# Optimization experiments

Measured on AMD Instinct MI355X. Metric: run time of the kernel, lower is better.

The kernel has to match this reference:

```python
import jax, jax.numpy as jnp
import numpy as np

D = 1024      # embedding_dimension
F = 4096      # intermediate_dimension
E = 8         # num_experts
K = 2         # top_k
B, S = 4, 2048


def setup_inputs() -> dict:
    key = jax.random.key(0)
    ks = jax.random.split(key, 6)
    scale_in = 1.0 / np.sqrt(D)
    scale_mid = 1.0 / np.sqrt(F)
    return {
        "x": jax.random.normal(ks[0], (B, S, D), dtype=jnp.float32),
        "router_w": jax.random.normal(ks[1], (E, D), dtype=jnp.float32) * scale_in,   # nn.Linear weight [out,in]
        "w1": jax.random.normal(ks[2], (E, F, D), dtype=jnp.float32) * scale_in,
        "b1": jax.random.normal(ks[3], (E, F), dtype=jnp.float32) * 0.01,
        "w2": jax.random.normal(ks[4], (E, D, F), dtype=jnp.float32) * scale_mid,
        "b2": jax.random.normal(ks[5], (E, D), dtype=jnp.float32) * 0.01,
    }


def reference(x, router_w, w1, b1, w2, b2):
    orig_shape = x.shape
    xf = x.reshape(-1, D)                                  # [T, D]
    logits = jnp.einsum("td,ed->te", xf, router_w)        # [T, E]
    top_vals, top_idx = jax.lax.top_k(logits, K)           # [T, K]
    probs = jax.nn.softmax(top_vals, axis=-1)              # [T, K]

    out = jnp.zeros_like(xf)
    for e in range(E):  # small fixed expert loop; masked dense combine
        # combine weight per token for expert e (0 if not routed)
        w = jnp.sum(jnp.where(top_idx == e, probs, 0.0), axis=-1)   # [T]
        h = jax.nn.gelu(jnp.einsum("td,fd->tf", xf, w1[e]) + b1[e], approximate=False)
        y = jnp.einsum("tf,df->td", h, w2[e]) + b2[e]
        out = out + w[:, None] * y
    return out.reshape(orig_shape)
```

## Files before the change

kernel.cpp:

```cpp
#include <hip/hip_runtime.h>
#include <hip/hip_bf16.h>
#include <stdint.h>

#define D 1024
#define F 4096
#define E 8
#define T 8192
#define SLOT_CAP 17408
#define BM 128
#define BK 32
#define EP_STRIDE 136

typedef __attribute__((ext_vector_type(8))) short bf16x8;
typedef __attribute__((ext_vector_type(4))) float f32x4;
typedef __attribute__((ext_vector_type(8))) unsigned short u16x8;

__device__ __forceinline__ unsigned short f2bf(float f) {
  unsigned u = __float_as_uint(f);
  u += 0x7fffu + ((u >> 16) & 1u);
  return (unsigned short)(u >> 16);
}
__device__ __forceinline__ float bf2f(unsigned short u) {
  return __uint_as_float(((unsigned)u) << 16);
}

__device__ __forceinline__ float gelu_f(float v) {
  float s = fabsf(v) * 0.70710678118654752f;
  float t = __builtin_amdgcn_rcpf(fmaf(0.3275911f, s, 1.0f));
  float p = fmaf(t, 1.061405429f, -1.453152027f);
  p = fmaf(t, p, 1.421413741f);
  p = fmaf(t, p, -0.284496736f);
  p = fmaf(t, p, 0.254829592f);
  p = p * t;
  float e = 1.0f - p * __expf(-s * s);
  e = copysignf(e, v);
  return 0.5f * v * (1.0f + e);
}

__device__ __forceinline__ void gload16(const void* g, void* l) {
  auto gp = (const __attribute__((address_space(1))) unsigned int*)(uintptr_t)g;
  auto lp = (__attribute__((address_space(3))) unsigned int*)(unsigned)(uintptr_t)l;
  __builtin_amdgcn_global_load_lds(gp, lp, 16, 0, 0);
}

__global__ __launch_bounds__(256) void prep_kernel(const float* __restrict__ x,
                                                   const float* __restrict__ rw,
                                                   const float* __restrict__ w1,
                                                   int* __restrict__ tok_e,
                                                   float* __restrict__ tok_p,
                                                   unsigned short* __restrict__ xg,
                                                   unsigned short* __restrict__ w1g) {
  if (blockIdx.x >= 2048) {
    int i = (blockIdx.x - 2048) * 256 + threadIdx.x;
    const float4* p = (const float4*)w1 + (size_t)i * 2;
    float4 a = p[0], b = p[1];
    u16x8 o;
    o[0] = f2bf(a.x); o[1] = f2bf(a.y); o[2] = f2bf(a.z); o[3] = f2bf(a.w);
    o[4] = f2bf(b.x); o[5] = f2bf(b.y); o[6] = f2bf(b.z); o[7] = f2bf(b.w);
    *(u16x8*)(w1g + (size_t)i * 8) = o;
    return;
  }
  int t = blockIdx.x * 4 + (threadIdx.x >> 6);
  int lane = threadIdx.x & 63;
  const float* xp = x + (size_t)t * D;
  unsigned short* xgp = xg + (size_t)t * D;
  double acc[E];
#pragma unroll
  for (int e = 0; e < E; e++) acc[e] = 0.0;
  for (int j = 0; j < D / 64; j++) {
    float xv = xp[j * 64 + lane];
    xgp[j * 64 + lane] = f2bf(xv);
#pragma unroll
    for (int e = 0; e < E; e++) acc[e] += (double)xv * (double)rw[e * D + j * 64 + lane];
  }
#pragma unroll
  for (int e = 0; e < E; e++) {
#pragma unroll
    for (int off = 32; off >= 1; off >>= 1) acc[e] += __shfl_xor(acc[e], off, 64);
  }
  if (lane == 0) {
    double v0 = -1e300, v1 = -1e300;
    int i0 = 0, i1 = 0;
#pragma unroll
    for (int e = 0; e < E; e++) {
      double v = acc[e];
      if (v > v0) { v1 = v0; i1 = i0; v0 = v; i0 = e; }
      else if (v > v1) { v1 = v; i1 = e; }
    }
    double e1 = exp(v1 - v0);
    double s = 1.0 + e1;
    tok_e[2 * t] = i0; tok_e[2 * t + 1] = i1;
    tok_p[2 * t] = (float)(1.0 / s);
    tok_p[2 * t + 1] = (float)(e1 / s);
  }
}

__global__ __launch_bounds__(64) void bucket_kernel(const int* __restrict__ tok_e,
                                                    int* __restrict__ perm,
                                                    int* __restrict__ slot_of,
                                                    int* __restrict__ counts,
                                                    int* __restrict__ offp) {
  const int e = blockIdx.x;
  const int lane = threadIdx.x;
  int cnt[E];
#pragma unroll
  for (int ee = 0; ee < E; ee++) cnt[ee] = 0;
  for (int idx = lane; idx < 2 * T; idx += 64) {
    int v = tok_e[idx];
#pragma unroll
    for (int ee = 0; ee < E; ee++) cnt[ee] += (v == ee) ? 1 : 0;
  }
#pragma unroll
  for (int ee = 0; ee < E; ee++) {
#pragma unroll
    for (int off = 32; off >= 1; off >>= 1) cnt[ee] += __shfl_xor(cnt[ee], off, 64);
  }
  int off_e[E + 1];
  int o = 0;
#pragma unroll
  for (int ee = 0; ee < E; ee++) { off_e[ee] = o; o += (cnt[ee] + (BM - 1)) & ~(BM - 1); }
  off_e[E] = o;
  if (e == 0 && lane == 0) {
#pragma unroll
    for (int ee = 0; ee < E; ee++) { counts[ee] = cnt[ee]; offp[ee] = off_e[ee]; }
    offp[E] = o;
  }
  int base = 0, mycnt = 0, myend = 0;
#pragma unroll
  for (int ee = 0; ee < E; ee++) {
    if (ee == e) { base = off_e[ee]; mycnt = cnt[ee]; myend = off_e[ee + 1]; }
  }
  const int pad0 = base + mycnt;
  for (int r = 0; r < 2 * T / 64; r++) {
    int idx = r * 64 + lane;
    int v = tok_e[idx];
    bool m = (v == e);
    unsigned long long mask = __ballot(m);
    int pre = __popcll(mask & ((1ull << lane) - 1ull));
    if (m) {
      int slot = base + pre;
      perm[slot] = idx >> 1;
      slot_of[idx] = slot;
    }
    base += __popcll(mask);
  }
  for (int i = pad0 + lane; i < myend; i += 64) perm[i] = 0;
}

__global__ __launch_bounds__(256, 4) void gemm1_kernel(const unsigned short* __restrict__ xg,
                                                       const unsigned short* __restrict__ w1g,
                                                       const float* __restrict__ b1,
                                                       const int* __restrict__ perm,
                                                       const int* __restrict__ offp,
                                                       const int* __restrict__ counts,
                                                       unsigned short* __restrict__ hbuf,
                                                       const float* __restrict__ w2,
                                                       unsigned short* __restrict__ w2g) {
  const int id = blockIdx.x;
  if (id >= 4352) {
    int i = (id - 4352) * 256 + threadIdx.x;
    const float4* p = (const float4*)w2 + (size_t)i * 2;
    float4 a = p[0], b = p[1];
    u16x8 o;
    o[0] = f2bf(a.x); o[1] = f2bf(a.y); o[2] = f2bf(a.z); o[3] = f2bf(a.w);
    o[4] = f2bf(b.x); o[5] = f2bf(b.y); o[6] = f2bf(b.z); o[7] = f2bf(b.w);
    *(u16x8*)(w2g + (size_t)i * 8) = o;
    return;
  }
  const int xcd = id & 7, loc = id >> 3;
  const int q = loc / 136, r = loc % 136;
  const int bm = xcd * 17 + (r >> 3);
  const int bn = q * 8 + (r & 7);
  const int row0 = bm * BM;
  if (row0 >= offp[E]) return;
  int e = 0;
#pragma unroll
  for (int i = 0; i < E; i++) if (row0 >= offp[i + 1]) e = i + 1;
  if (row0 >= offp[e] + counts[e]) return;

  const int tid = threadIdx.x, lane = tid & 63, w = tid >> 6;
  __shared__ __align__(16) unsigned short smem[BM * EP_STRIDE];
  unsigned short* As0 = smem;
  unsigned short* Bs0 = smem + 8192;

  const unsigned short* gsrc[4];
  unsigned short* ldst[4];
#pragma unroll
  for (int i = 0; i < 4; i++) {
    int ch = tid + 256 * i;
    if (ch < 512) {
      int ar = ch >> 2, ac = (ch & 3) * 8;
      gsrc[i] = xg + (size_t)perm[row0 + ar] * D + ac;
      ldst[i] = As0 + ch * 8;
    } else {
      int c = ch - 512;
      int br = c >> 2, bc = (c & 3) * 8;
      gsrc[i] = w1g + ((size_t)e * F + (size_t)bn * BM + br) * D + bc;
      ldst[i] = Bs0 + c * 8;
    }
  }
  auto stage = [&](int k0, int buf) {
#pragma unroll
    for (int i = 0; i < 4; i++) gload16(gsrc[i] + k0, ldst[i] + buf * (BM * BK));
  };

  f32x4 acc[4][4] = {};
  const int wr = (w >> 1) * 64, wc = (w & 1) * 64;
  const int fr = lane & 15, fq = lane >> 4;

  stage(0, 0);
  __syncthreads();
  int cur = 0;
  for (int k0 = 0; k0 < D; k0 += BK) {
    if (k0 + BK < D) stage(k0 + BK, cur ^ 1);
    bf16x8 a[4], b[4];
#pragma unroll
    for (int m = 0; m < 4; m++) a[m] = *(const bf16x8*)&As0[cur * 4096 + (wr + m * 16 + fr) * BK + fq * 8];
#pragma unroll
    for (int n = 0; n < 4; n++) b[n] = *(const bf16x8*)&Bs0[cur * 4096 + (wc + n * 16 + fr) * BK + fq * 8];
#pragma unroll
    for (int m = 0; m < 4; m++)
#pragma unroll
      for (int n = 0; n < 4; n++)
        acc[m][n] = __builtin_amdgcn_mfma_f32_16x16x32_bf16(a[m], b[n], acc[m][n], 0, 0, 0);
    __syncthreads();
    cur ^= 1;
  }

#pragma unroll
  for (int n = 0; n < 4; n++) {
    int cl = wc + n * 16 + fr;
    float bias = b1[e * F + bn * BM + cl];
#pragma unroll
    for (int m = 0; m < 4; m++) {
#pragma unroll
      for (int j = 0; j < 4; j++) {
        int rl = wr + m * 16 + fq * 4 + j;
        smem[rl * EP_STRIDE + cl] = f2bf(gelu_f(acc[m][n][j] + bias));
      }
    }
  }
  __syncthreads();
#pragma unroll
  for (int i = 0; i < 8; i++) {
    int idx = tid + i * 256;
    int r2 = idx >> 4, c = (idx & 15) * 8;
    u16x8 v = *(const u16x8*)&smem[r2 * EP_STRIDE + c];
    *(u16x8*)&hbuf[(size_t)(row0 + r2) * F + bn * BM + c] = v;
  }
}

__global__ __launch_bounds__(256, 4) void gemm2_kernel(const unsigned short* __restrict__ hbuf,
                                                       const unsigned short* __restrict__ w2g,
                                                       const float* __restrict__ b2,
                                                       const int* __restrict__ offp,
                                                       const int* __restrict__ counts,
                                                       unsigned short* __restrict__ ypart) {
  const int id = blockIdx.x;
  const int swz = (id & 7) * 272 + (id >> 3);
  const int bn = swz & 7;
  const int ks = (swz >> 3) & 1;
  const int bm = swz >> 4;
  const int row0 = bm * BM;
  if (row0 >= offp[E]) return;
  int e = 0;
#pragma unroll
  for (int i = 0; i < E; i++) if (row0 >= offp[i + 1]) e = i + 1;
  const int valid_end = offp[e] + counts[e];
  if (row0 >= valid_end) return;

  const int tid = threadIdx.x, lane = tid & 63, w = tid >> 6;
  __shared__ __align__(16) unsigned short smem[BM * EP_STRIDE];
  unsigned short* As0 = smem;
  unsigned short* Bs0 = smem + 8192;

  const int kbase = ks * (F / 2);
  const unsigned short* gsrc[4];
  unsigned short* ldst[4];
#pragma unroll
  for (int i = 0; i < 4; i++) {
    int ch = tid + 256 * i;
    if (ch < 512) {
      int ar = ch >> 2, ac = (ch & 3) * 8;
      gsrc[i] = hbuf + (size_t)(row0 + ar) * F + kbase + ac;
      ldst[i] = As0 + ch * 8;
    } else {
      int c = ch - 512;
      int br = c >> 2, bc = (c & 3) * 8;
      gsrc[i] = w2g + ((size_t)e * D + (size_t)bn * BM + br) * F + kbase + bc;
      ldst[i] = Bs0 + c * 8;
    }
  }
  auto stage = [&](int k0, int buf) {
#pragma unroll
    for (int i = 0; i < 4; i++) gload16(gsrc[i] + k0, ldst[i] + buf * (BM * BK));
  };

  f32x4 acc[4][4] = {};
  const int wr = (w >> 1) * 64, wc = (w & 1) * 64;
  const int fr = lane & 15, fq = lane >> 4;

  stage(0, 0);
  __syncthreads();
  int cur = 0;
  for (int k0 = 0; k0 < F / 2; k0 += BK) {
    if (k0 + BK < F / 2) stage(k0 + BK, cur ^ 1);
    bf16x8 a[4], b[4];
#pragma unroll
    for (int m = 0; m < 4; m++) a[m] = *(const bf16x8*)&As0[cur * 4096 + (wr + m * 16 + fr) * BK + fq * 8];
#pragma unroll
    for (int n = 0; n < 4; n++) b[n] = *(const bf16x8*)&Bs0[cur * 4096 + (wc + n * 16 + fr) * BK + fq * 8];
#pragma unroll
    for (int m = 0; m < 4; m++)
#pragma unroll
      for (int n = 0; n < 4; n++)
        acc[m][n] = __builtin_amdgcn_mfma_f32_16x16x32_bf16(a[m], b[n], acc[m][n], 0, 0, 0);
    __syncthreads();
    cur ^= 1;
  }

#pragma unroll
  for (int n = 0; n < 4; n++) {
    int cl = wc + n * 16 + fr;
    float bias = (ks == 0) ? b2[e * D + bn * BM + cl] : 0.0f;
#pragma unroll
    for (int m = 0; m < 4; m++) {
#pragma unroll
      for (int j = 0; j < 4; j++) {
        int rl = wr + m * 16 + fq * 4 + j;
        smem[rl * EP_STRIDE + cl] = f2bf(acc[m][n][j] + bias);
      }
    }
  }
  __syncthreads();
  unsigned short* ybase = ypart + (size_t)ks * SLOT_CAP * D;
#pragma unroll
  for (int i = 0; i < 8; i++) {
    int idx = tid + i * 256;
    int r2 = idx >> 4, c = (idx & 15) * 8;
    if (row0 + r2 < valid_end) {
      u16x8 v = *(const u16x8*)&smem[r2 * EP_STRIDE + c];
      *(u16x8*)&ybase[(size_t)(row0 + r2) * D + bn * BM + c] = v;
    }
  }
}

__global__ __launch_bounds__(256) void combine_kernel(const unsigned short* __restrict__ ypart,
                                                      const int* __restrict__ slot_of,
                                                      const float* __restrict__ tok_p,
                                                      float* __restrict__ out) {
  int i = blockIdx.x * 256 + threadIdx.x;
  int t = i >> 7;
  int g8 = i & 127;
  int s0 = slot_of[2 * t], s1 = slot_of[2 * t + 1];
  float g0 = tok_p[2 * t], g1 = tok_p[2 * t + 1];
  const unsigned short* p0 = ypart;
  const unsigned short* p1 = ypart + (size_t)SLOT_CAP * D;
  u16x8 a0 = *(const u16x8*)(p0 + (size_t)s0 * D + g8 * 8);
  u16x8 b0 = *(const u16x8*)(p1 + (size_t)s0 * D + g8 * 8);
  u16x8 a1 = *(const u16x8*)(p0 + (size_t)s1 * D + g8 * 8);
  u16x8 b1 = *(const u16x8*)(p1 + (size_t)s1 * D + g8 * 8);
  float o[8];
#pragma unroll
  for (int j = 0; j < 8; j++)
    o[j] = g0 * (bf2f(a0[j]) + bf2f(b0[j])) + g1 * (bf2f(a1[j]) + bf2f(b1[j]));
  float4* op = (float4*)(out + (size_t)t * D + g8 * 8);
  op[0] = make_float4(o[0], o[1], o[2], o[3]);
  op[1] = make_float4(o[4], o[5], o[6], o[7]);
}

extern "C" void kernel_launch(void* const* d_in, const int* in_sizes, int n_in,
                              void* d_out, int out_size, void* d_ws, size_t ws_size,
                              hipStream_t stream) {
  const float* x = (const float*)d_in[0];
  const float* rw = (const float*)d_in[1];
  const float* w1 = (const float*)d_in[2];
  const float* b1 = (const float*)d_in[3];
  const float* w2 = (const float*)d_in[4];
  const float* b2 = (const float*)d_in[5];
  float* out = (float*)d_out;

  char* ws = (char*)d_ws;
  size_t off = 0;
  auto alloc = [&](size_t bytes) {
    void* p = ws + off;
    off = (off + bytes + 255) & ~(size_t)255;
    return p;
  };
  int* counts = (int*)alloc(E * 4);
  int* offp = (int*)alloc((E + 1) * 4);
  int* tok_e = (int*)alloc((size_t)T * 2 * 4);
  float* tok_p = (float*)alloc((size_t)T * 2 * 4);
  int* perm = (int*)alloc((size_t)SLOT_CAP * 4);
  int* slot_of = (int*)alloc((size_t)T * 2 * 4);
  unsigned short* xg = (unsigned short*)alloc((size_t)T * D * 2);
  unsigned short* w1g = (unsigned short*)alloc((size_t)E * F * D * 2);
  unsigned short* w2g = (unsigned short*)alloc((size_t)E * D * F * 2);
  unsigned short* hbuf = (unsigned short*)alloc((size_t)SLOT_CAP * F * 2);
  unsigned short* ypart = xg;
  (void)ws_size; (void)in_sizes; (void)n_in; (void)out_size;

  hipLaunchKernelGGL(prep_kernel, dim3(2048 + E * F * D / 8 / 256), dim3(256), 0, stream,
                     x, rw, w1, tok_e, tok_p, xg, w1g);
  hipLaunchKernelGGL(bucket_kernel, dim3(E), dim3(64), 0, stream,
                     tok_e, perm, slot_of, counts, offp);
  hipLaunchKernelGGL(gemm1_kernel, dim3(4352 + E * D * F / 8 / 256), dim3(256), 0, stream,
                     xg, w1g, b1, perm, offp, counts, hbuf, w2, w2g);
  hipLaunchKernelGGL(gemm2_kernel, dim3(2176), dim3(256), 0, stream,
                     hbuf, w2g, b2, offp, counts, ypart);
  hipLaunchKernelGGL(combine_kernel, dim3(T * D / 8 / 256), dim3(256), 0, stream,
                     ypart, slot_of, tok_p, out);
}
```

Baseline: 553.7 us.

## Fuse w1 fp32-to-bf16 conversion into gemm1 B-tile loading

Removes the separate pass in prep_kernel that converted all of w1 to bf16 in a workspace buffer. gemm1 now loads fp32 w1 directly through registers, converts to bf16 and writes the B tile to LDS after the MFMAs, while A still uses direct global-to-LDS loads. This saves writing and re-reading a bf16 copy of w1, but each w1 tile is now read as fp32 and converted by every M-block that uses it, so global traffic and VGPR pressure in the GEMM rise. The fp32-to-bf16 conversions also switch to HIP's packed bf16 intrinsic.

```diff
diff --git a/kernel.cpp b/kernel.cpp
--- a/kernel.cpp
+++ b/kernel.cpp
@@ -22,6 +22,16 @@
 }
 __device__ __forceinline__ float bf2f(unsigned short u) {
   return __uint_as_float(((unsigned)u) << 16);
+}
+
+__device__ __forceinline__ u16x8 cvt8(float4 a, float4 b) {
+  __hip_bfloat162 p0 = __float22bfloat162_rn(make_float2(a.x, a.y));
+  __hip_bfloat162 p1 = __float22bfloat162_rn(make_float2(a.z, a.w));
+  __hip_bfloat162 p2 = __float22bfloat162_rn(make_float2(b.x, b.y));
+  __hip_bfloat162 p3 = __float22bfloat162_rn(make_float2(b.z, b.w));
+  union { __hip_bfloat162 h[4]; u16x8 v; } u;
+  u.h[0] = p0; u.h[1] = p1; u.h[2] = p2; u.h[3] = p3;
+  return u.v;
 }
 
 __device__ __forceinline__ float gelu_f(float v) {
@@ -45,21 +55,9 @@
 
 __global__ __launch_bounds__(256) void prep_kernel(const float* __restrict__ x,
                                                    const float* __restrict__ rw,
-                                                   const float* __restrict__ w1,
                                                    int* __restrict__ tok_e,
                                                    float* __restrict__ tok_p,
-                                                   unsigned short* __restrict__ xg,
-                                                   unsigned short* __restrict__ w1g) {
-  if (blockIdx.x >= 2048) {
-    int i = (blockIdx.x - 2048) * 256 + threadIdx.x;
-    const float4* p = (const float4*)w1 + (size_t)i * 2;
-    float4 a = p[0], b = p[1];
-    u16x8 o;
-    o[0] = f2bf(a.x); o[1] = f2bf(a.y); o[2] = f2bf(a.z); o[3] = f2bf(a.w);
-    o[4] = f2bf(b.x); o[5] = f2bf(b.y); o[6] = f2bf(b.z); o[7] = f2bf(b.w);
-    *(u16x8*)(w1g + (size_t)i * 8) = o;
-    return;
-  }
+                                                   unsigned short* __restrict__ xg) {
   int t = blockIdx.x * 4 + (threadIdx.x >> 6);
   int lane = threadIdx.x & 63;
   const float* xp = x + (size_t)t * D;
@@ -148,7 +146,7 @@
 }
 
 __global__ __launch_bounds__(256, 4) void gemm1_kernel(const unsigned short* __restrict__ xg,
-                                                       const unsigned short* __restrict__ w1g,
+                                                       const float* __restrict__ w1,
                                                        const float* __restrict__ b1,
                                                        const int* __restrict__ perm,
                                                        const int* __restrict__ offp,
@@ -161,10 +159,7 @@
     int i = (id - 4352) * 256 + threadIdx.x;
     const float4* p = (const float4*)w2 + (size_t)i * 2;
     float4 a = p[0], b = p[1];
-    u16x8 o;
-    o[0] = f2bf(a.x); o[1] = f2bf(a.y); o[2] = f2bf(a.z); o[3] = f2bf(a.w);
-    o[4] = f2bf(b.x); o[5] = f2bf(b.y); o[6] = f2bf(b.z); o[7] = f2bf(b.w);
-    *(u16x8*)(w2g + (size_t)i * 8) = o;
+    *(u16x8*)(w2g + (size_t)i * 8) = cvt8(a, b);
     return;
   }
   const int xcd = id & 7, loc = id >> 3;
@@ -183,36 +178,49 @@
   unsigned short* As0 = smem;
   unsigned short* Bs0 = smem + 8192;
 
-  const unsigned short* gsrc[4];
-  unsigned short* ldst[4];
-#pragma unroll
-  for (int i = 0; i < 4; i++) {
+  const unsigned short* asrc[2];
+  unsigned short* adst[2];
+#pragma unroll
+  for (int i = 0; i < 2; i++) {
     int ch = tid + 256 * i;
-    if (ch < 512) {
-      int ar = ch >> 2, ac = (ch & 3) * 8;
-      gsrc[i] = xg + (size_t)perm[row0 + ar] * D + ac;
-      ldst[i] = As0 + ch * 8;
-    } else {
-      int c = ch - 512;
-      int br = c >> 2, bc = (c & 3) * 8;
-      gsrc[i] = w1g + ((size_t)e * F + (size_t)bn * BM + br) * D + bc;
-      ldst[i] = Bs0 + c * 8;
-    }
-  }
-  auto stage = [&](int k0, int buf) {
-#pragma unroll
-    for (int i = 0; i < 4; i++) gload16(gsrc[i] + k0, ldst[i] + buf * (BM * BK));
+    int ar = ch >> 2, ac = (ch & 3) * 8;
+    asrc[i] = xg + (size_t)perm[row0 + ar] * D + ac;
+    adst[i] = As0 + ch * 8;
+  }
+  auto stageA = [&](int k0, int buf) {
+#pragma unroll
+    for (int i = 0; i < 2; i++) gload16(asrc[i] + k0, adst[i] + buf * (BM * BK));
   };
+
+  const int brow = tid >> 2, bpr = tid & 3;
+  const float* bsrc = w1 + ((size_t)e * F + (size_t)bn * BM + brow) * D + bpr * 8;
+  unsigned short* bdst = Bs0 + brow * 32 + bpr * 8;
 
   f32x4 acc[4][4] = {};
   const int wr = (w >> 1) * 64, wc = (w & 1) * 64;
   const int fr = lane & 15, fq = lane >> 4;
 
-  stage(0, 0);
+  {
+    float4 p0 = *(const float4*)(bsrc);
+    float4 p1 = *(const float4*)(bsrc + 4);
+    float4 p2 = *(const float4*)(bsrc + 64 * D);
+    float4 p3 = *(const float4*)(bsrc + 64 * D + 4);
+    *(u16x8*)(bdst) = cvt8(p0, p1);
+    *(u16x8*)(bdst + 2048) = cvt8(p2, p3);
+    stageA(0, 0);
+  }
   __syncthreads();
   int cur = 0;
   for (int k0 = 0; k0 < D; k0 += BK) {
-    if (k0 + BK < D) stage(k0 + BK, cur ^ 1);
+    const bool more = (k0 + BK < D);
+    float4 p0, p1, p2, p3;
+    if (more) {
+      p0 = *(const float4*)(bsrc + k0 + BK);
+      p1 = *(const float4*)(bsrc + k0 + BK + 4);
+      p2 = *(const float4*)(bsrc + 64 * D + k0 + BK);
+      p3 = *(const float4*)(bsrc + 64 * D + k0 + BK + 4);
+      stageA(k0 + BK, cur ^ 1);
+    }
     bf16x8 a[4], b[4];
 #pragma unroll
     for (int m = 0; m < 4; m++) a[m] = *(const bf16x8*)&As0[cur * 4096 + (wr + m * 16 + fr) * BK + fq * 8];
@@ -223,6 +231,11 @@
 #pragma unroll
       for (int n = 0; n < 4; n++)
         acc[m][n] = __builtin_amdgcn_mfma_f32_16x16x32_bf16(a[m], b[n], acc[m][n], 0, 0, 0);
+    if (more) {
+      unsigned short* d = bdst + (cur ^ 1) * 4096;
+      *(u16x8*)(d) = cvt8(p0, p1);
+      *(u16x8*)(d + 2048) = cvt8(p2, p3);
+    }
     __syncthreads();
     cur ^= 1;
   }
@@ -394,18 +407,18 @@
   int* perm = (int*)alloc((size_t)SLOT_CAP * 4);
   int* slot_of = (int*)alloc((size_t)T * 2 * 4);
   unsigned short* xg = (unsigned short*)alloc((size_t)T * D * 2);
-  unsigned short* w1g = (unsigned short*)alloc((size_t)E * F * D * 2);
+  unsigned short* ydead = (unsigned short*)alloc((size_t)E * F * D * 2);
   unsigned short* w2g = (unsigned short*)alloc((size_t)E * D * F * 2);
   unsigned short* hbuf = (unsigned short*)alloc((size_t)SLOT_CAP * F * 2);
   unsigned short* ypart = xg;
-  (void)ws_size; (void)in_sizes; (void)n_in; (void)out_size;
-
-  hipLaunchKernelGGL(prep_kernel, dim3(2048 + E * F * D / 8 / 256), dim3(256), 0, stream,
-                     x, rw, w1, tok_e, tok_p, xg, w1g);
+  (void)ydead; (void)ws_size; (void)in_sizes; (void)n_in; (void)out_size;
+
+  hipLaunchKernelGGL(prep_kernel, dim3(2048), dim3(256), 0, stream,
+                     x, rw, tok_e, tok_p, xg);
   hipLaunchKernelGGL(bucket_kernel, dim3(E), dim3(64), 0, stream,
                      tok_e, perm, slot_of, counts, offp);
   hipLaunchKernelGGL(gemm1_kernel, dim3(4352 + E * D * F / 8 / 256), dim3(256), 0, stream,
-                     xg, w1g, b1, perm, offp, counts, hbuf, w2, w2g);
+                     xg, w1, b1, perm, offp, counts, hbuf, w2, w2g);
   hipLaunchKernelGGL(gemm2_kernel, dim3(2176), dim3(256), 0, stream,
                      hbuf, w2g, b2, offp, counts, ypart);
   hipLaunchKernelGGL(combine_kernel, dim3(T * D / 8 / 256), dim3(256), 0, stream,
```

Result: slower. 595.4 us (+7.5%).
